# Kernel optimization log

Measured on AMD Instinct MI355X. Metric: run time of the kernel, lower is better.

## Reference

```python
import jax, jax.numpy as jnp
import numpy as np

B, S, D = 4, 2048, 1024
H, DK, DV = 16, 64, 64
LN_EPS = 1e-5


def setup_inputs() -> dict:
    key = jax.random.key(0)
    ks = jax.random.split(key, 6)
    x = jax.random.normal(ks[0], (B, S, D), dtype=jnp.float32)
    # causal mask: True = masked position (j > i), broadcast over batch
    causal = jnp.triu(jnp.ones((S, S), dtype=bool), k=1)
    attention_mask = jnp.broadcast_to(causal, (B, S, S))
    scale = 1.0 / np.sqrt(D)
    w_q = jax.random.normal(ks[1], (D, H * DK), dtype=jnp.float32) * scale
    w_k = jax.random.normal(ks[2], (D, H * DK), dtype=jnp.float32) * scale
    w_v = jax.random.normal(ks[3], (D, H * DV), dtype=jnp.float32) * scale
    w_fc = jax.random.normal(ks[4], (H * DV, D), dtype=jnp.float32) * (1.0 / np.sqrt(H * DV))
    ln_gamma = jnp.ones((D,), dtype=jnp.float32)
    ln_beta = jnp.zeros((D,), dtype=jnp.float32)
    return {"x": x, "attention_mask": attention_mask, "w_q": w_q, "w_k": w_k,
            "w_v": w_v, "w_fc": w_fc, "ln_gamma": ln_gamma, "ln_beta": ln_beta}


def _layernorm(y, gamma, beta):
    mu = jnp.mean(y, axis=-1, keepdims=True)
    var = jnp.mean(jnp.square(y - mu), axis=-1, keepdims=True)
    return (y - mu) * jax.lax.rsqrt(var + LN_EPS) * gamma + beta


def reference(x, attention_mask, w_q, w_k, w_v, w_fc, ln_gamma, ln_beta):
    b, s, _ = x.shape
    # projections -> [b, h, s, dk/dv]
    q = (x @ w_q).reshape(b, s, H, DK).transpose(0, 2, 1, 3)
    k = (x @ w_k).reshape(b, s, H, DK).transpose(0, 2, 1, 3)
    v = (x @ w_v).reshape(b, s, H, DV).transpose(0, 2, 1, 3)
    # scaled dot-product attention with mask (True -> -1e9)
    scores = jnp.einsum('bhqd,bhkd->bhqk', q, k) / np.sqrt(DK)
    scores = jnp.where(attention_mask[:, None, :, :], jnp.float32(-1e9), scores)
    attn = jax.nn.softmax(scores, axis=-1)
    context = jnp.einsum('bhqk,bhkd->bhqd', attn, v)
    context = context.transpose(0, 2, 1, 3).reshape(b, s, H * DV)
    output = context @ w_fc
    out = _layernorm(output + x, ln_gamma, ln_beta)
    return out, attn
```

## Files before the change

kernel.cpp:

```cpp
#include <hip/hip_runtime.h>
#include <stdint.h>

#define S_LEN 2048
#define NHEAD 16

typedef short short8 __attribute__((ext_vector_type(8)));
typedef float f32x4 __attribute__((ext_vector_type(4)));
typedef unsigned short u16;

typedef __attribute__((address_space(1))) uint32_t AS1u32;
typedef __attribute__((address_space(3))) uint32_t AS3u32;

#define MFMA16(a, b, c) __builtin_amdgcn_mfma_f32_16x16x32_bf16((a), (b), (c), 0, 0, 0)

__device__ __forceinline__ void gload16(const void* g, void* l) {
  __builtin_amdgcn_global_load_lds((AS1u32*)g, (AS3u32*)l, 16, 0, 0);
}

__device__ __forceinline__ u16 f2bf(float f) {
  union { float f; uint32_t u; } c; c.f = f;
  return (u16)((c.u + 0x7fffu + ((c.u >> 16) & 1u)) >> 16);
}
__device__ __forceinline__ float bf2f(u16 h) {
  union { uint32_t u; float f; } c; c.u = ((uint32_t)h) << 16;
  return c.f;
}

__global__ __launch_bounds__(256) void conv_x_kernel(const float* __restrict__ x,
                                                     u16* __restrict__ xb) {
  size_t i = ((size_t)blockIdx.x * 256 + threadIdx.x) * 4;
  f32x4 v = *(const f32x4*)(x + i);
  union { u16 h[4]; uint2 d; } o;
  o.h[0] = f2bf(v[0]); o.h[1] = f2bf(v[1]); o.h[2] = f2bf(v[2]); o.h[3] = f2bf(v[3]);
  *(uint2*)(xb + i) = o.d;
}

__global__ __launch_bounds__(256) void transpose_w_kernel(
    const float* __restrict__ w0, const float* __restrict__ w1,
    const float* __restrict__ w2, const float* __restrict__ w3,
    u16* __restrict__ qkvT, u16* __restrict__ fcT) {
  int z = blockIdx.z;
  const float* w = (z == 0) ? w0 : (z == 1) ? w1 : (z == 2) ? w2 : w3;
  u16* o = (z == 3) ? fcT : qkvT + (size_t)z * 1048576;
  float scale = (z == 0) ? 0.125f : 1.0f;
  __shared__ float t[32][33];
  int n0 = blockIdx.x * 32, k0 = blockIdx.y * 32;
  int tx = threadIdx.x & 31, ty = threadIdx.x >> 5;
#pragma unroll
  for (int i = 0; i < 4; ++i) {
    int k = ty * 4 + i;
    t[k][tx] = w[(size_t)(k0 + k) * 1024 + n0 + tx];
  }
  __syncthreads();
#pragma unroll
  for (int i = 0; i < 4; ++i) {
    int n = ty * 4 + i;
    o[(size_t)(n0 + n) * 1024 + k0 + tx] = f2bf(t[tx][n] * scale);
  }
}

__device__ __forceinline__ void gemm_stage(const char* Ab, const char* Bb, u16* As, u16* Bs,
                                           int m0, int n0, int kbyte, int tid) {
#pragma unroll
  for (int i = 0; i < 2; ++i) {
    int cid = i * 256 + tid;
    int row = cid >> 2, c = cid & 3;
    int off = kbyte + ((c ^ ((row >> 1) & 3)) << 4);
    gload16(Ab + (size_t)(m0 + row) * 2048 + off, (char*)As + i * 4096 + (tid & ~63) * 16);
    gload16(Bb + (size_t)(n0 + row) * 2048 + off, (char*)Bs + i * 4096 + (tid & ~63) * 16);
  }
}

__global__ __launch_bounds__(256) void gemm_bt_kernel(
    const u16* __restrict__ A, const u16* __restrict__ BT,
    void* __restrict__ out, int mode) {
  __shared__ u16 As[128 * 32];
  __shared__ u16 Bs[128 * 32];
  const int tid = threadIdx.x;
  const int lane = tid & 63, wv = tid >> 6;
  const int l15 = lane & 15, h16 = lane >> 4;
  const int wr = wv >> 1, wc = wv & 1;
  const int m0 = blockIdx.x * 128, n0 = blockIdx.y * 128;
  const char* Ab = (const char*)A;
  const char* Bb = (const char*)BT;

  f32x4 acc[4][4];
#pragma unroll
  for (int i = 0; i < 4; ++i)
#pragma unroll
    for (int j = 0; j < 4; ++j) acc[i][j] = (f32x4){0.f, 0.f, 0.f, 0.f};

  gemm_stage(Ab, Bb, As, Bs, m0, n0, 0, tid);
  for (int kt = 0; kt < 32; ++kt) {
    __syncthreads();
    short8 a[4], b[4];
#pragma unroll
    for (int mf = 0; mf < 4; ++mf) {
      int row = wr * 64 + mf * 16 + l15;
      a[mf] = *(const short8*)((const char*)As + row * 64 + ((h16 ^ ((row >> 1) & 3)) << 4));
    }
#pragma unroll
    for (int nf = 0; nf < 4; ++nf) {
      int row = wc * 64 + nf * 16 + l15;
      b[nf] = *(const short8*)((const char*)Bs + row * 64 + ((h16 ^ ((row >> 1) & 3)) << 4));
    }
#pragma unroll
    for (int mf = 0; mf < 4; ++mf)
#pragma unroll
      for (int nf = 0; nf < 4; ++nf)
        acc[mf][nf] = MFMA16(a[mf], b[nf], acc[mf][nf]);
    __syncthreads();
    if (kt + 1 < 32) gemm_stage(Ab, Bb, As, Bs, m0, n0, (kt + 1) * 64, tid);
  }

  if (mode == 0) {
    u16* o = (u16*)out;
#pragma unroll
    for (int mf = 0; mf < 4; ++mf)
#pragma unroll
      for (int nf = 0; nf < 4; ++nf)
#pragma unroll
        for (int r = 0; r < 4; ++r) {
          int m = m0 + wr * 64 + mf * 16 + 4 * h16 + r;
          int n = n0 + wc * 64 + nf * 16 + l15;
          int z = n >> 10, nn = n & 1023;
          int bb = m >> 11, s = m & 2047, hh = nn >> 6, dk = nn & 63;
          o[(size_t)z * 8388608 + (((size_t)(bb * NHEAD + hh) * S_LEN + s) << 6) + dk] =
              f2bf(acc[mf][nf][r]);
        }
  } else {
    float* o = (float*)out;
#pragma unroll
    for (int mf = 0; mf < 4; ++mf)
#pragma unroll
      for (int nf = 0; nf < 4; ++nf)
#pragma unroll
        for (int r = 0; r < 4; ++r) {
          int m = m0 + wr * 64 + mf * 16 + 4 * h16 + r;
          int n = n0 + wc * 64 + nf * 16 + l15;
          o[(size_t)m * 1024 + n] = acc[mf][nf][r];
        }
  }
}

__global__ __launch_bounds__(256) void transpose_v_kernel(
    const u16* __restrict__ v, u16* __restrict__ vT) {
  __shared__ u16 t[64][80];
  int bh = blockIdx.y, s0 = blockIdx.x * 64;
  int tid = threadIdx.x;
  int sl = tid >> 2, c = tid & 3;
  const u16* src = v + (size_t)bh * S_LEN * 64 + (size_t)(s0 + sl) * 64 + c * 16;
  short8 a = *(const short8*)src;
  short8 b = *(const short8*)(src + 8);
#pragma unroll
  for (int j = 0; j < 8; ++j) {
    t[c * 16 + j][sl] = (u16)a[j];
    t[c * 16 + 8 + j][sl] = (u16)b[j];
  }
  __syncthreads();
  int dv = tid >> 2, c2 = tid & 3;
  u16* dst = vT + (size_t)bh * 64 * S_LEN + (size_t)dv * S_LEN + s0 + c2 * 16;
  *(short8*)dst = *(const short8*)&t[dv][c2 * 16];
  *(short8*)(dst + 8) = *(const short8*)&t[dv][c2 * 16 + 8];
}

__device__ __forceinline__ void stage_qk(const char* base, int row0, u16* dst, int tid) {
#pragma unroll
  for (int i = 0; i < 2; ++i) {
    int cid = i * 512 + tid;
    int row = cid >> 3, c = cid & 7;
    gload16(base + (size_t)(row0 + row) * 128 + ((c ^ (row & 7)) << 4),
            (char*)dst + i * 8192 + (tid & ~63) * 16);
  }
}
__device__ __forceinline__ void stage_v(const char* Vb, int kv0, u16* dst, int tid) {
#pragma unroll
  for (int i = 0; i < 2; ++i) {
    int cid = i * 512 + tid;
    int row = cid >> 4, c = cid & 15;
    gload16(Vb + (size_t)row * 4096 + (size_t)kv0 * 2 + ((c ^ (row & 7)) << 4),
            (char*)dst + i * 8192 + (tid & ~63) * 16);
  }
}

__global__ __launch_bounds__(512) void denom_kernel(
    const u16* __restrict__ Q, const u16* __restrict__ K, float* __restrict__ rinv) {
  __shared__ u16 Qs[128 * 64];
  __shared__ u16 Ks[2][128 * 64];
  const int tid = threadIdx.x;
  const int lane = tid & 63, wv = tid >> 6;
  const int l15 = lane & 15, h16 = lane >> 4;
  const int w16 = wv * 16;
  const int qt = blockIdx.x, bh = blockIdx.y;
  const int q0 = qt * 128;
  const char* Qb = (const char*)(Q + (size_t)bh * S_LEN * 64);
  const char* Kb = (const char*)(K + (size_t)bh * S_LEN * 64);

  stage_qk(Qb, q0, Qs, tid);
  stage_qk(Kb, 0, Ks[0], tid);
  __syncthreads();
  short8 qf[2];
  {
    int row = w16 + l15;
    qf[0] = *(const short8*)((const char*)Qs + row * 128 + ((h16 ^ (row & 7)) << 4));
    qf[1] = *(const short8*)((const char*)Qs + row * 128 + (((4 + h16) ^ (row & 7)) << 4));
  }
  __syncthreads();

  float lsum[4] = {0.f, 0.f, 0.f, 0.f};
  int cur = 0;
  for (int t = 0; t <= qt; ++t) {
    if (t + 1 <= qt) stage_qk(Kb, (t + 1) * 128, Ks[cur ^ 1], tid);
    const char* Kc = (const char*)Ks[cur];
    f32x4 sc[8];
#pragma unroll
    for (int nf = 0; nf < 8; ++nf) sc[nf] = (f32x4){0.f, 0.f, 0.f, 0.f};
#pragma unroll
    for (int ks = 0; ks < 2; ++ks)
#pragma unroll
      for (int nf = 0; nf < 8; ++nf) {
        int row = nf * 16 + l15;
        short8 kb = *(const short8*)(Kc + row * 128 + (((ks * 4 + h16) ^ (row & 7)) << 4));
        sc[nf] = MFMA16(qf[ks], kb, sc[nf]);
      }
    if (t == qt) {
#pragma unroll
      for (int nf = 0; nf < 8; ++nf)
#pragma unroll
        for (int r = 0; r < 4; ++r)
          if (nf * 16 + l15 > w16 + 4 * h16 + r) sc[nf][r] = -1e30f;
    }
#pragma unroll
    for (int nf = 0; nf < 8; ++nf)
#pragma unroll
      for (int r = 0; r < 4; ++r) lsum[r] += __expf(sc[nf][r]);
    __syncthreads();
    cur ^= 1;
  }
#pragma unroll
  for (int r = 0; r < 4; ++r) {
    float v = lsum[r];
    v += __shfl_xor(v, 1);
    v += __shfl_xor(v, 2);
    v += __shfl_xor(v, 4);
    v += __shfl_xor(v, 8);
    lsum[r] = v;
  }
  if (l15 == 0) {
    f32x4 o = {1.f / lsum[0], 1.f / lsum[1], 1.f / lsum[2], 1.f / lsum[3]};
    *(f32x4*)(rinv + (size_t)bh * S_LEN + q0 + w16 + 4 * h16) = o;
  }
}

__global__ __launch_bounds__(512) void emit_kernel(
    const u16* __restrict__ Q, const u16* __restrict__ K, const u16* __restrict__ VT,
    const float* __restrict__ rinv, float* __restrict__ attn, u16* __restrict__ ctx) {
  __shared__ u16 Ks[2][128 * 64];
  __shared__ u16 Vs[64 * 128];
  __shared__ u16 Ps[128 * 128];

  const int tid = threadIdx.x;
  const int lane = tid & 63, wv = tid >> 6;
  const int l15 = lane & 15, h16 = lane >> 4;
  const int w16 = wv * 16;
  const int qt = blockIdx.x, bh = blockIdx.y;
  const int q0 = qt * 128;

  const char* Qb = (const char*)(Q + (size_t)bh * S_LEN * 64);
  const char* Kb = (const char*)(K + (size_t)bh * S_LEN * 64);
  const char* Vb = (const char*)(VT + (size_t)bh * 64 * S_LEN);
  float* attb = attn + (size_t)bh * S_LEN * S_LEN;

  stage_qk(Qb, q0, Ps, tid);
  stage_qk(Kb, 0, Ks[0], tid);
  __syncthreads();
  short8 qf[2];
  {
    int row = w16 + l15;
    qf[0] = *(const short8*)((const char*)Ps + row * 128 + ((h16 ^ (row & 7)) << 4));
    qf[1] = *(const short8*)((const char*)Ps + row * 128 + (((4 + h16) ^ (row & 7)) << 4));
  }
  f32x4 ri = *(const f32x4*)(rinv + (size_t)bh * S_LEN + q0 + w16 + 4 * h16);
  __syncthreads();

  f32x4 cacc[4];
#pragma unroll
  for (int nf = 0; nf < 4; ++nf) cacc[nf] = (f32x4){0.f, 0.f, 0.f, 0.f};

  int cur = 0;
  for (int t = 0; t <= qt; ++t) {
    const int kv0 = t * 128;
    stage_v(Vb, kv0, Vs, tid);
    const char* Kc = (const char*)Ks[cur];
    f32x4 sc[8];
#pragma unroll
    for (int nf = 0; nf < 8; ++nf) sc[nf] = (f32x4){0.f, 0.f, 0.f, 0.f};
#pragma unroll
    for (int ks = 0; ks < 2; ++ks)
#pragma unroll
      for (int nf = 0; nf < 8; ++nf) {
        int row = nf * 16 + l15;
        short8 kb = *(const short8*)(Kc + row * 128 + (((ks * 4 + h16) ^ (row & 7)) << 4));
        sc[nf] = MFMA16(qf[ks], kb, sc[nf]);
      }
    if (t == qt) {
#pragma unroll
      for (int nf = 0; nf < 8; ++nf)
#pragma unroll
        for (int r = 0; r < 4; ++r)
          if (nf * 16 + l15 > w16 + 4 * h16 + r) sc[nf][r] = -1e30f;
    }
#pragma unroll
    for (int nf = 0; nf < 8; ++nf)
#pragma unroll
      for (int r = 0; r < 4; ++r) {
        float p = __expf(sc[nf][r]) * ri[r];
        int rowL = w16 + 4 * h16 + r;
        int chunk = 2 * nf + (l15 >> 3);
        *(u16*)((char*)Ps + rowL * 256 + ((chunk ^ (rowL & 7)) << 4) + (l15 & 7) * 2) = f2bf(p);
      }
    __syncthreads();
    if (t + 1 <= qt) stage_qk(Kb, kv0 + 128, Ks[cur ^ 1], tid);
#pragma unroll
    for (int ks = 0; ks < 4; ++ks) {
      int rowP = w16 + l15;
      short8 pa = *(const short8*)((const char*)Ps + rowP * 256 + (((ks * 4 + h16) ^ (rowP & 7)) << 4));
#pragma unroll
      for (int nf = 0; nf < 4; ++nf) {
        int rowV = nf * 16 + l15;
        short8 vbf = *(const short8*)((const char*)Vs + rowV * 256 + (((ks * 4 + h16) ^ (rowV & 7)) << 4));
        cacc[nf] = MFMA16(pa, vbf, cacc[nf]);
      }
    }
    {
      int row = tid >> 2, sub = tid & 3;
      const char* prow = (const char*)Ps + row * 256;
      float* arow = attb + (size_t)(q0 + row) * S_LEN + kv0;
#pragma unroll
      for (int c8 = 0; c8 < 4; ++c8) {
        int chunk = sub + 4 * c8;
        short8 pv = *(const short8*)(prow + ((chunk ^ (row & 7)) << 4));
        f32x4 f0 = {bf2f((u16)pv[0]), bf2f((u16)pv[1]), bf2f((u16)pv[2]), bf2f((u16)pv[3])};
        f32x4 f1 = {bf2f((u16)pv[4]), bf2f((u16)pv[5]), bf2f((u16)pv[6]), bf2f((u16)pv[7])};
        *(f32x4*)(arow + chunk * 8) = f0;
        *(f32x4*)(arow + chunk * 8 + 4) = f1;
      }
    }
    __syncthreads();
    cur ^= 1;
  }

  for (int kvt = qt + 1; kvt < 16; ++kvt) {
    const int kv0 = kvt * 128;
    int row = tid >> 2, sub = tid & 3;
    float* arow = attb + (size_t)(q0 + row) * S_LEN + kv0;
    f32x4 z = {0.f, 0.f, 0.f, 0.f};
#pragma unroll
    for (int c8 = 0; c8 < 4; ++c8) {
      int chunk = sub + 4 * c8;
      *(f32x4*)(arow + chunk * 8) = z;
      *(f32x4*)(arow + chunk * 8 + 4) = z;
    }
  }

  {
    int b = bh >> 4, hh = bh & 15;
#pragma unroll
    for (int nf = 0; nf < 4; ++nf)
#pragma unroll
      for (int r = 0; r < 4; ++r) {
        int qrow = q0 + w16 + 4 * h16 + r;
        ctx[((size_t)b * S_LEN + qrow) * 1024 + hh * 64 + nf * 16 + l15] = f2bf(cacc[nf][r]);
      }
  }
}

__global__ __launch_bounds__(256) void ln_kernel(float* __restrict__ io,
                                                 const float* __restrict__ x,
                                                 const float* __restrict__ gamma,
                                                 const float* __restrict__ beta) {
  int row = blockIdx.x, tid = threadIdx.x;
  size_t base = (size_t)row * 1024 + tid * 4;
  f32x4 p = *(const f32x4*)(io + base);
  f32x4 xv = *(const f32x4*)(x + base);
  f32x4 y;
  float s1 = 0.f, s2 = 0.f;
#pragma unroll
  for (int j = 0; j < 4; ++j) {
    y[j] = p[j] + xv[j];
    s1 += y[j];
    s2 += y[j] * y[j];
  }
#pragma unroll
  for (int off = 1; off <= 32; off <<= 1) {
    s1 += __shfl_xor(s1, off);
    s2 += __shfl_xor(s2, off);
  }
  __shared__ float r1[4], r2[4];
  int w = tid >> 6;
  if ((tid & 63) == 0) { r1[w] = s1; r2[w] = s2; }
  __syncthreads();
  float S1 = r1[0] + r1[1] + r1[2] + r1[3];
  float S2 = r2[0] + r2[1] + r2[2] + r2[3];
  float mu = S1 * (1.f / 1024.f);
  float var = S2 * (1.f / 1024.f) - mu * mu;
  float rs = rsqrtf(var + 1e-5f);
  f32x4 g = *(const f32x4*)(gamma + tid * 4);
  f32x4 bt = *(const f32x4*)(beta + tid * 4);
  f32x4 o;
#pragma unroll
  for (int j = 0; j < 4; ++j) o[j] = (y[j] - mu) * rs * g[j] + bt[j];
  *(f32x4*)(io + base) = o;
}

extern "C" void kernel_launch(void* const* d_in, const int* in_sizes, int n_in,
                              void* d_out, int out_size, void* d_ws, size_t ws_size,
                              hipStream_t stream) {
  (void)in_sizes; (void)n_in; (void)out_size; (void)ws_size;
  const float* x = (const float*)d_in[0];
  const float* wq = (const float*)d_in[2];
  const float* wk = (const float*)d_in[3];
  const float* wv = (const float*)d_in[4];
  const float* wfc = (const float*)d_in[5];
  const float* gamma = (const float*)d_in[6];
  const float* beta = (const float*)d_in[7];

  char* ws = (char*)d_ws;
  u16* xb = (u16*)ws;
  u16* wqkvT = (u16*)(ws + (16u << 20));
  u16* wfcT = (u16*)(ws + (22u << 20));
  u16* qkvb = (u16*)(ws + (24u << 20));
  u16* qb = qkvb;
  u16* kb = qkvb + (size_t)8388608;
  u16* vb = qkvb + (size_t)16777216;
  u16* vT = (u16*)(ws + (72u << 20));
  float* rinvp = (float*)(ws + (56u << 20));
  u16* ctx = xb;

  float* outp = (float*)d_out;
  float* attnp = outp + (size_t)4 * 2048 * 1024;

  conv_x_kernel<<<8192, 256, 0, stream>>>(x, xb);
  transpose_w_kernel<<<dim3(32, 32, 4), 256, 0, stream>>>(wq, wk, wv, wfc, wqkvT, wfcT);
  gemm_bt_kernel<<<dim3(64, 24), 256, 0, stream>>>(xb, wqkvT, qkvb, 0);
  transpose_v_kernel<<<dim3(32, 64), 256, 0, stream>>>(vb, vT);
  denom_kernel<<<dim3(16, 64), 512, 0, stream>>>(qb, kb, rinvp);
  emit_kernel<<<dim3(16, 64), 512, 0, stream>>>(qb, kb, vT, rinvp, attnp, ctx);
  gemm_bt_kernel<<<dim3(64, 8), 256, 0, stream>>>(ctx, wfcT, outp, 1);
  ln_kernel<<<8192, 256, 0, stream>>>(outp, x, gamma, beta);
}
```

Before: 480.2 us.

## Merge prep kernels, stage QKV epilogue via LDS, and schedule heavy causal tiles first

After: 487.3 us. About the same (+1.5%).

```diff
diff --git a/kernel.cpp b/kernel.cpp
--- a/kernel.cpp
+++ b/kernel.cpp
@@ -26,25 +26,28 @@
   return c.f;
 }
 
-__global__ __launch_bounds__(256) void conv_x_kernel(const float* __restrict__ x,
-                                                     u16* __restrict__ xb) {
-  size_t i = ((size_t)blockIdx.x * 256 + threadIdx.x) * 4;
-  f32x4 v = *(const f32x4*)(x + i);
-  union { u16 h[4]; uint2 d; } o;
-  o.h[0] = f2bf(v[0]); o.h[1] = f2bf(v[1]); o.h[2] = f2bf(v[2]); o.h[3] = f2bf(v[3]);
-  *(uint2*)(xb + i) = o.d;
-}
-
-__global__ __launch_bounds__(256) void transpose_w_kernel(
+__global__ __launch_bounds__(256) void prep_kernel(
+    const float* __restrict__ x, u16* __restrict__ xb,
     const float* __restrict__ w0, const float* __restrict__ w1,
     const float* __restrict__ w2, const float* __restrict__ w3,
     u16* __restrict__ qkvT, u16* __restrict__ fcT) {
-  int z = blockIdx.z;
+  __shared__ float t[32][33];
+  int bid = blockIdx.x;
+  if (bid < 8192) {
+    size_t i = ((size_t)bid * 256 + threadIdx.x) * 4;
+    f32x4 v = *(const f32x4*)(x + i);
+    union { u16 h[4]; uint2 d; } o;
+    o.h[0] = f2bf(v[0]); o.h[1] = f2bf(v[1]); o.h[2] = f2bf(v[2]); o.h[3] = f2bf(v[3]);
+    *(uint2*)(xb + i) = o.d;
+    return;
+  }
+  int r = bid - 8192;
+  int z = r >> 10; r &= 1023;
+  int bx = r & 31, by = r >> 5;
   const float* w = (z == 0) ? w0 : (z == 1) ? w1 : (z == 2) ? w2 : w3;
   u16* o = (z == 3) ? fcT : qkvT + (size_t)z * 1048576;
   float scale = (z == 0) ? 0.125f : 1.0f;
-  __shared__ float t[32][33];
-  int n0 = blockIdx.x * 32, k0 = blockIdx.y * 32;
+  int n0 = bx * 32, k0 = by * 32;
   int tx = threadIdx.x & 31, ty = threadIdx.x >> 5;
 #pragma unroll
   for (int i = 0; i < 4; ++i) {
@@ -74,8 +77,9 @@
 __global__ __launch_bounds__(256) void gemm_bt_kernel(
     const u16* __restrict__ A, const u16* __restrict__ BT,
     void* __restrict__ out, int mode) {
-  __shared__ u16 As[128 * 32];
-  __shared__ u16 Bs[128 * 32];
+  __shared__ u16 sh[128 * 128];
+  u16* As = sh;
+  u16* Bs = sh + 4096;
   const int tid = threadIdx.x;
   const int lane = tid & 63, wv = tid >> 6;
   const int l15 = lane & 15, h16 = lane >> 4;
@@ -121,13 +125,24 @@
       for (int nf = 0; nf < 4; ++nf)
 #pragma unroll
         for (int r = 0; r < 4; ++r) {
-          int m = m0 + wr * 64 + mf * 16 + 4 * h16 + r;
-          int n = n0 + wc * 64 + nf * 16 + l15;
-          int z = n >> 10, nn = n & 1023;
-          int bb = m >> 11, s = m & 2047, hh = nn >> 6, dk = nn & 63;
-          o[(size_t)z * 8388608 + (((size_t)(bb * NHEAD + hh) * S_LEN + s) << 6) + dk] =
+          int row = wr * 64 + mf * 16 + 4 * h16 + r;
+          int col = wc * 64 + nf * 16 + l15;
+          *(u16*)((char*)sh + row * 256 + (((col >> 3) ^ (row & 7)) << 4) + (col & 7) * 2) =
               f2bf(acc[mf][nf][r]);
         }
+    __syncthreads();
+    int row = tid >> 1, hf = tid & 1;
+    int m = m0 + row;
+    int bb = m >> 11, s = m & 2047;
+    int n_base = n0 + hf * 64;
+    int z = n_base >> 10, nn = n_base & 1023, hh = nn >> 6;
+    u16* dst = o + (size_t)z * 8388608 + (((size_t)(bb * NHEAD + hh) * S_LEN + s) << 6);
+#pragma unroll
+    for (int i = 0; i < 8; ++i) {
+      int ch = hf * 8 + i;
+      short8 v = *(const short8*)((const char*)sh + row * 256 + ((ch ^ (row & 7)) << 4));
+      *(short8*)(dst + i * 8) = v;
+    }
   } else {
     float* o = (float*)out;
 #pragma unroll
@@ -191,7 +206,7 @@
   const int lane = tid & 63, wv = tid >> 6;
   const int l15 = lane & 15, h16 = lane >> 4;
   const int w16 = wv * 16;
-  const int qt = blockIdx.x, bh = blockIdx.y;
+  const int qt = 15 - blockIdx.x, bh = blockIdx.y;
   const int q0 = qt * 128;
   const char* Qb = (const char*)(Q + (size_t)bh * S_LEN * 64);
   const char* Kb = (const char*)(K + (size_t)bh * S_LEN * 64);
@@ -263,7 +278,7 @@
   const int lane = tid & 63, wv = tid >> 6;
   const int l15 = lane & 15, h16 = lane >> 4;
   const int w16 = wv * 16;
-  const int qt = blockIdx.x, bh = blockIdx.y;
+  const int qt = 15 - blockIdx.x, bh = blockIdx.y;
   const int q0 = qt * 128;
 
   const char* Qb = (const char*)(Q + (size_t)bh * S_LEN * 64);
@@ -440,8 +455,7 @@
   float* outp = (float*)d_out;
   float* attnp = outp + (size_t)4 * 2048 * 1024;
 
-  conv_x_kernel<<<8192, 256, 0, stream>>>(x, xb);
-  transpose_w_kernel<<<dim3(32, 32, 4), 256, 0, stream>>>(wq, wk, wv, wfc, wqkvT, wfcT);
+  prep_kernel<<<12288, 256, 0, stream>>>(x, xb, wq, wk, wv, wfc, wqkvT, wfcT);
   gemm_bt_kernel<<<dim3(64, 24), 256, 0, stream>>>(xb, wqkvT, qkvb, 0);
   transpose_v_kernel<<<dim3(32, 64), 256, 0, stream>>>(vb, vT);
   denom_kernel<<<dim3(16, 64), 512, 0, stream>>>(qb, kb, rinvp);
```
